# Optimization experiments

Hardware: AMD Instinct MI355X
Metric: run time of the kernel (lower is better)

The kernel has to match this reference:

```python
import jax, jax.numpy as jnp
import numpy as np

TAU = 0.01
MASK_VALUE = -1000000.0


def setup_inputs() -> dict:
    key = jax.random.key(0)
    kq, kk, km, k1, k2, k3 = jax.random.split(key, 6)
    B, Lq, Lk = 4, 512, 512
    Dq = Dk = 256
    H = 128
    queries = jax.random.normal(kq, (B, Lq, Dq), dtype=jnp.float32)
    keys = jax.random.normal(kk, (B, Lk, Dk), dtype=jnp.float32)
    # valid length along the size-2 logits axis, in {1, 2}
    mask = jax.random.randint(km, (B, Lq, Lk), 1, 3, dtype=jnp.int32)
    Wq = jax.random.normal(k1, (H, Dq), dtype=jnp.float32) * 0.05
    Wk = jax.random.normal(k2, (H, Dk), dtype=jnp.float32) * 0.05
    Wv = jax.random.normal(k3, (2, H), dtype=jnp.float32) * 0.05
    return {"queries": queries, "keys": keys, "mask": mask,
            "Wq": Wq, "Wk": Wk, "Wv": Wv}


def reference(queries, keys, mask, Wq, Wk, Wv):
    # Linear projections (no bias): [B,Lq,H], [B,Lk,H]
    q = jnp.einsum('bqd,hd->bqh', queries, Wq)
    k = jnp.einsum('bkd,hd->bkh', keys, Wk)
    # Bahdanau broadcast-add + tanh: [B,Lq,Lk,H]
    features = jnp.tanh(q[:, :, None, :] + k[:, None, :, :])
    # Project to 2 logits: [B,Lq,Lk,2]
    scores = jnp.einsum('bqkh,ch->bqkc', features, Wv)
    # sequence_mask along the size-2 last axis: positions >= valid_len get -1e6
    pos = jnp.arange(2, dtype=mask.dtype)
    masked = jnp.where(pos < mask[..., None], scores, MASK_VALUE)
    # Gumbel-softmax (soft), tau=0.01, over last axis; take channel 0
    g = jax.random.gumbel(jax.random.key(42), masked.shape, dtype=masked.dtype)
    weights = jax.nn.softmax((masked + g) / TAU, axis=-1)
    return weights[..., 0]
```

## Files before the change

### kernel.cpp

```cpp
#include <hip/hip_runtime.h>
#include <stdint.h>


#define BB 4
#define LLEN 512
#define DD 256
#define HH 128

#define TWO_LOG2E 2.8853900817779268f
#define LOG2E_100 144.26950408889634f

#define NWAVES 2048
#define REGION 512

__device__ __forceinline__ uint32_t rotl32(uint32_t v, int r) {
  return __builtin_amdgcn_alignbit(v, v, 32 - r);
}

__device__ __forceinline__ void tf2x32(uint32_t x0, uint32_t x1,
                                       uint32_t& o0, uint32_t& o1) {
  const uint32_t k0 = 0u;
  const uint32_t k1 = 42u;
  const uint32_t k2 = 0x1BD11BDAu ^ k0 ^ k1;

  x0 += k0; x1 += k1;
#define TFR(r) { x0 += x1; x1 = rotl32(x1, (r)); x1 ^= x0; }
  TFR(13) TFR(15) TFR(26) TFR(6)
  x0 += k1; x1 += k2 + 1u;
  TFR(17) TFR(29) TFR(16) TFR(24)
  x0 += k2; x1 += k0 + 2u;
  TFR(13) TFR(15) TFR(26) TFR(6)
  x0 += k0; x1 += k1 + 3u;
  TFR(17) TFR(29) TFR(16) TFR(24)
  x0 += k1; x1 += k2 + 4u;
  TFR(13) TFR(15) TFR(26) TFR(6)
  x0 += k2; x1 += k0 + 5u;
#undef TFR
  o0 = x0; o1 = x1;
}

__device__ __forceinline__ float jax_u01(uint32_t flat) {
  uint32_t o0, o1;
  tf2x32(0u, flat, o0, o1);
  const uint32_t bits = o0 ^ o1;
  const float f = __uint_as_float((bits >> 9) | 0x3F800000u) - 1.0f;
  return fmaxf(f, 1.17549435e-38f);
}

__global__ __launch_bounds__(128) void proj_kernel(
    const float* __restrict__ queries, const float* __restrict__ keys,
    const float* __restrict__ Wq, const float* __restrict__ Wk,
    float* __restrict__ EQ, float* __restrict__ EK) {
  const int blk = blockIdx.x;
  const bool isK = blk >= 512;
  const int rb = (isK ? blk - 512 : blk) * 4;
  const float* __restrict__ in = isK ? keys : queries;
  const float* __restrict__ W  = isK ? Wk : Wq;
  float* __restrict__ outp     = isK ? EK : EQ;

  __shared__ float rows[4][DD];
  const float4* in4 = reinterpret_cast<const float4*>(in + (size_t)rb * DD);
  float4* rows4 = reinterpret_cast<float4*>(&rows[0][0]);
  #pragma unroll
  for (int t = threadIdx.x; t < 4 * DD / 4; t += 128) rows4[t] = in4[t];
  __syncthreads();

  const int h = threadIdx.x;
  const float4* W4 = reinterpret_cast<const float4*>(W + (size_t)h * DD);
  float a0 = 0.f, a1 = 0.f, a2 = 0.f, a3 = 0.f;
  #pragma unroll 8
  for (int d4 = 0; d4 < DD / 4; ++d4) {
    const float4 w = W4[d4];
    const int d = d4 * 4;
    a0 = fmaf(w.x, rows[0][d], fmaf(w.y, rows[0][d+1], fmaf(w.z, rows[0][d+2], fmaf(w.w, rows[0][d+3], a0))));
    a1 = fmaf(w.x, rows[1][d], fmaf(w.y, rows[1][d+1], fmaf(w.z, rows[1][d+2], fmaf(w.w, rows[1][d+3], a1))));
    a2 = fmaf(w.x, rows[2][d], fmaf(w.y, rows[2][d+1], fmaf(w.z, rows[2][d+2], fmaf(w.w, rows[2][d+3], a2))));
    a3 = fmaf(w.x, rows[3][d], fmaf(w.y, rows[3][d+1], fmaf(w.z, rows[3][d+2], fmaf(w.w, rows[3][d+3], a3))));
  }
  float* orow = outp + (size_t)rb * HH + h;
  orow[0 * HH] = __builtin_amdgcn_exp2f(a0 * TWO_LOG2E);
  orow[1 * HH] = __builtin_amdgcn_exp2f(a1 * TWO_LOG2E);
  orow[2 * HH] = __builtin_amdgcn_exp2f(a2 * TWO_LOG2E);
  orow[3 * HH] = __builtin_amdgcn_exp2f(a3 * TWO_LOG2E);
}

#define GRP(accv, qv, kv, wd) {                                       \
    float4 A_;                                                        \
    A_.x = fmaf((qv).x, (kv).x, 1.0f);                                \
    A_.y = fmaf((qv).y, (kv).y, 1.0f);                                \
    A_.z = fmaf((qv).z, (kv).z, 1.0f);                                \
    A_.w = fmaf((qv).w, (kv).w, 1.0f);                                \
    const float p01_ = A_.x * A_.y;                                   \
    const float p23_ = A_.z * A_.w;                                   \
    const float n01_ = fmaf((wd).x, A_.y, (wd).y * A_.x);             \
    const float n23_ = fmaf((wd).z, A_.w, (wd).w * A_.z);             \
    const float num_ = fmaf(n01_, p23_, n23_ * p01_);                 \
    const float rc_  = __builtin_amdgcn_rcpf(p01_ * p23_);            \
    (accv) = fmaf(num_, rc_, (accv)); }

__global__ __launch_bounds__(256) void attn_loop(
    const float* __restrict__ EQ, const float* __restrict__ EK,
    const int* __restrict__ mask, const float* __restrict__ Wv,
    float* __restrict__ out, uint32_t* __restrict__ counts,
    uint2* __restrict__ entbuf) {
  __shared__ float4 QL[32][33];
  __shared__ float4 KL[64][33];
  __shared__ float4 wdL[32];

  const int bi = blockIdx.x, bj = blockIdx.y, b = blockIdx.z;
  const int i0 = bi * 32, j0 = bj * 64;

  const float4* Q4 = reinterpret_cast<const float4*>(EQ) + ((size_t)b * LLEN + i0) * (HH / 4);
  const float4* K4 = reinterpret_cast<const float4*>(EK) + ((size_t)b * LLEN + j0) * (HH / 4);
  for (int t = threadIdx.x; t < 1024 + 2048; t += 256) {
    if (t < 1024) {
      QL[t >> 5][t & 31] = Q4[t];
    } else {
      const int u = t - 1024;
      KL[u >> 5][u & 31] = K4[u];
    }
  }
  if (threadIdx.x < 32) {
    const float4 w0 = reinterpret_cast<const float4*>(Wv)[threadIdx.x];
    const float4 w1 = reinterpret_cast<const float4*>(Wv)[32 + threadIdx.x];
    float4 wd; wd.x = w0.x - w1.x; wd.y = w0.y - w1.y;
    wd.z = w0.z - w1.z; wd.w = w0.w - w1.w;
    wdL[threadIdx.x] = wd;
  }
  __syncthreads();

  const int jj = threadIdx.x & 31;
  const int ib = threadIdx.x >> 5;

  const uint32_t row0 = (uint32_t)b * LLEN + i0 + ib;
  const uint32_t col0 = j0 + jj;
  int mreg[4][2];
  #pragma unroll
  for (int r = 0; r < 4; ++r)
    #pragma unroll
    for (int c = 0; c < 2; ++c)
      mreg[r][c] = mask[(row0 + 8u * r) * LLEN + col0 + 32u * c];

  float Swd = 0.f;
  #pragma unroll
  for (int t = 0; t < 32; ++t) {
    const float4 wd = wdL[t];
    Swd += (wd.x + wd.y) + (wd.z + wd.w);
  }

  float acc[4][2] = {{0.f,0.f},{0.f,0.f},{0.f,0.f},{0.f,0.f}};

  #pragma unroll 4
  for (int h4 = 0; h4 < HH / 4; ++h4) {
    const float4 kv0 = KL[jj][h4];
    const float4 kv1 = KL[jj + 32][h4];
    const float4 wd  = wdL[h4];
    const float4 qv0 = QL[ib][h4];
    const float4 qv1 = QL[ib + 8][h4];
    const float4 qv2 = QL[ib + 16][h4];
    const float4 qv3 = QL[ib + 24][h4];
    GRP(acc[0][0], qv0, kv0, wd) GRP(acc[0][1], qv0, kv1, wd)
    GRP(acc[1][0], qv1, kv0, wd) GRP(acc[1][1], qv1, kv1, wd)
    GRP(acc[2][0], qv2, kv0, wd) GRP(acc[2][1], qv2, kv1, wd)
    GRP(acc[3][0], qv3, kv0, wd) GRP(acc[3][1], qv3, kv1, wd)
  }

  const int lane = threadIdx.x & 63;
  const unsigned long long lanemask_lt = (1ull << lane) - 1ull;
  const uint32_t wave_id =
      (((uint32_t)blockIdx.z * gridDim.y + blockIdx.y) * gridDim.x + blockIdx.x) * 4u
      + (threadIdx.x >> 6);
  uint2* __restrict__ reg = entbuf + (size_t)wave_id * REGION;

  uint32_t off = 0;
  #pragma unroll
  for (int r = 0; r < 4; ++r) {
    #pragma unroll
    for (int c = 0; c < 2; ++c) {
      const uint32_t idx = (row0 + 8u * r) * LLEN + col0 + 32u * c;
      const bool need = (mreg[r][c] >= 2);
      const unsigned long long bal = __ballot(need);
      if (need) {
        const uint32_t rank = (uint32_t)__popcll(bal & lanemask_lt);
        uint2 ent;
        ent.x = idx;
        ent.y = __float_as_uint(fmaf(-2.0f, acc[r][c], Swd));
        reg[off + rank] = ent;
      } else {
        out[idx] = 1.0f;
      }
      off += (uint32_t)__popcll(bal);
    }
  }
  if (lane == 0) counts[wave_id] = off;
}

__global__ __launch_bounds__(256) void attn_epi(
    const uint32_t* __restrict__ counts, const uint2* __restrict__ entbuf,
    float* __restrict__ out) {
  const int lane = threadIdx.x & 63;
  const uint32_t g = (uint32_t)blockIdx.x * 4u + (threadIdx.x >> 6);
  const uint32_t cnt = counts[g];
  if (cnt == 0) return;
  const uint2* __restrict__ reg = entbuf + (size_t)g * REGION;

  const int iters = (int)((cnt + 63u) >> 6);
  #pragma unroll 2
  for (int k = 0; k < iters; ++k) {
    const uint32_t e = (uint32_t)k * 64u + (uint32_t)lane;
    const bool valid = e < cnt;
    const uint32_t eL = valid ? e : (cnt - 1u);
    const uint2 ent = reg[eL];

    const float dv = __uint_as_float(ent.y);
    const float l0 = __log2f(jax_u01(ent.x * 2u));
    const float l1 = __log2f(jax_u01(ent.x * 2u + 1u));
    const float rl = l1 * __builtin_amdgcn_rcpf(l0);
    const float dl = __log2f(rl);
    const float t  = fmaf(dv, LOG2E_100, 100.0f * dl);
    const float o  = __builtin_amdgcn_rcpf(1.0f + __builtin_amdgcn_exp2f(-t));
    if (valid) out[ent.x] = o;
  }
}

extern "C" void kernel_launch(void* const* d_in, const int* in_sizes, int n_in,
                              void* d_out, int out_size, void* d_ws, size_t ws_size,
                              hipStream_t stream) {
  const float* queries = (const float*)d_in[0];
  const float* keys    = (const float*)d_in[1];
  const int*   mask    = (const int*)d_in[2];
  const float* Wq      = (const float*)d_in[3];
  const float* Wk      = (const float*)d_in[4];
  const float* Wv      = (const float*)d_in[5];
  float* out = (float*)d_out;

  float* EQ = (float*)d_ws;
  float* EK = EQ + (size_t)BB * LLEN * HH;
  uint32_t* counts = (uint32_t*)(EK + (size_t)BB * LLEN * HH);
  uint2* entbuf = (uint2*)((char*)counts + 16384);

  proj_kernel<<<dim3(1024), dim3(128), 0, stream>>>(
      queries, keys, Wq, Wk, EQ, EK);
  attn_loop<<<dim3(LLEN / 32, LLEN / 64, BB), dim3(256), 0, stream>>>(
      EQ, EK, mask, Wv, out, counts, entbuf);
  attn_epi<<<dim3(NWAVES / 4), dim3(256), 0, stream>>>(
      counts, entbuf, out);
}
```

Measured before the change: 47.22 us.

## Precompute Gumbel noise in the projection kernel and drop the compaction epilogue

Gumbel noise log terms for all sites are now computed in extra blocks of the projection kernel and written to a workspace buffer. The attention kernel reads that buffer alongside the mask and computes the final sigmoid inline, which removes the ballot/compaction scatter and the third epilogue launch. In exchange, threefry hashing now runs for every site rather than only the roughly half whose mask is 2. It also adds a 4 MB write and a 4 MB read of noise values.

Result: faster. 42.13 us (-10.8%).

```diff
diff --git a/kernel.cpp b/kernel.cpp
--- a/kernel.cpp
+++ b/kernel.cpp
@@ -10,8 +10,8 @@
 #define TWO_LOG2E 2.8853900817779268f
 #define LOG2E_100 144.26950408889634f
 
-#define NWAVES 2048
-#define REGION 512
+#define NSITES (BB * LLEN * LLEN)
+#define GUMBEL_THREADS (NSITES / 2)
 
 __device__ __forceinline__ uint32_t rotl32(uint32_t v, int r) {
   return __builtin_amdgcn_alignbit(v, v, 32 - r);
@@ -47,11 +47,25 @@
   return fmaxf(f, 1.17549435e-38f);
 }
 
-__global__ __launch_bounds__(128) void proj_kernel(
+__global__ __launch_bounds__(128) void prep_kernel(
     const float* __restrict__ queries, const float* __restrict__ keys,
     const float* __restrict__ Wq, const float* __restrict__ Wk,
-    float* __restrict__ EQ, float* __restrict__ EK) {
+    float* __restrict__ EQ, float* __restrict__ EK, float* __restrict__ G) {
   const int blk = blockIdx.x;
+
+  if (blk >= 1024) {
+    const uint32_t base = (uint32_t)(blk - 1024) * 128u + threadIdx.x;
+    #pragma unroll
+    for (int rep = 0; rep < 2; ++rep) {
+      const uint32_t s = base + (uint32_t)rep * GUMBEL_THREADS;
+      const float l0 = __log2f(jax_u01(s * 2u));
+      const float l1 = __log2f(jax_u01(s * 2u + 1u));
+      const float rl = l1 * __builtin_amdgcn_rcpf(l0);
+      G[s] = 100.0f * __log2f(rl);
+    }
+    return;
+  }
+
   const bool isK = blk >= 512;
   const int rb = (isK ? blk - 512 : blk) * 4;
   const float* __restrict__ in = isK ? keys : queries;
@@ -98,11 +112,10 @@
     const float rc_  = __builtin_amdgcn_rcpf(p01_ * p23_);            \
     (accv) = fmaf(num_, rc_, (accv)); }
 
-__global__ __launch_bounds__(256) void attn_loop(
+__global__ __launch_bounds__(256) void attn_kernel(
     const float* __restrict__ EQ, const float* __restrict__ EK,
     const int* __restrict__ mask, const float* __restrict__ Wv,
-    float* __restrict__ out, uint32_t* __restrict__ counts,
-    uint2* __restrict__ entbuf) {
+    const float* __restrict__ G, float* __restrict__ out) {
   __shared__ float4 QL[32][33];
   __shared__ float4 KL[64][33];
   __shared__ float4 wdL[32];
@@ -134,12 +147,16 @@
 
   const uint32_t row0 = (uint32_t)b * LLEN + i0 + ib;
   const uint32_t col0 = j0 + jj;
-  int mreg[4][2];
+  int   mreg[4][2];
+  float greg[4][2];
   #pragma unroll
   for (int r = 0; r < 4; ++r)
     #pragma unroll
-    for (int c = 0; c < 2; ++c)
-      mreg[r][c] = mask[(row0 + 8u * r) * LLEN + col0 + 32u * c];
+    for (int c = 0; c < 2; ++c) {
+      const uint32_t idx = (row0 + 8u * r) * LLEN + col0 + 32u * c;
+      mreg[r][c] = mask[idx];
+      greg[r][c] = G[idx];
+    }
 
   float Swd = 0.f;
   #pragma unroll
@@ -165,61 +182,16 @@
     GRP(acc[3][0], qv3, kv0, wd) GRP(acc[3][1], qv3, kv1, wd)
   }
 
-  const int lane = threadIdx.x & 63;
-  const unsigned long long lanemask_lt = (1ull << lane) - 1ull;
-  const uint32_t wave_id =
-      (((uint32_t)blockIdx.z * gridDim.y + blockIdx.y) * gridDim.x + blockIdx.x) * 4u
-      + (threadIdx.x >> 6);
-  uint2* __restrict__ reg = entbuf + (size_t)wave_id * REGION;
-
-  uint32_t off = 0;
   #pragma unroll
   for (int r = 0; r < 4; ++r) {
     #pragma unroll
     for (int c = 0; c < 2; ++c) {
       const uint32_t idx = (row0 + 8u * r) * LLEN + col0 + 32u * c;
-      const bool need = (mreg[r][c] >= 2);
-      const unsigned long long bal = __ballot(need);
-      if (need) {
-        const uint32_t rank = (uint32_t)__popcll(bal & lanemask_lt);
-        uint2 ent;
-        ent.x = idx;
-        ent.y = __float_as_uint(fmaf(-2.0f, acc[r][c], Swd));
-        reg[off + rank] = ent;
-      } else {
-        out[idx] = 1.0f;
-      }
-      off += (uint32_t)__popcll(bal);
-    }
-  }
-  if (lane == 0) counts[wave_id] = off;
-}
-
-__global__ __launch_bounds__(256) void attn_epi(
-    const uint32_t* __restrict__ counts, const uint2* __restrict__ entbuf,
-    float* __restrict__ out) {
-  const int lane = threadIdx.x & 63;
-  const uint32_t g = (uint32_t)blockIdx.x * 4u + (threadIdx.x >> 6);
-  const uint32_t cnt = counts[g];
-  if (cnt == 0) return;
-  const uint2* __restrict__ reg = entbuf + (size_t)g * REGION;
-
-  const int iters = (int)((cnt + 63u) >> 6);
-  #pragma unroll 2
-  for (int k = 0; k < iters; ++k) {
-    const uint32_t e = (uint32_t)k * 64u + (uint32_t)lane;
-    const bool valid = e < cnt;
-    const uint32_t eL = valid ? e : (cnt - 1u);
-    const uint2 ent = reg[eL];
-
-    const float dv = __uint_as_float(ent.y);
-    const float l0 = __log2f(jax_u01(ent.x * 2u));
-    const float l1 = __log2f(jax_u01(ent.x * 2u + 1u));
-    const float rl = l1 * __builtin_amdgcn_rcpf(l0);
-    const float dl = __log2f(rl);
-    const float t  = fmaf(dv, LOG2E_100, 100.0f * dl);
-    const float o  = __builtin_amdgcn_rcpf(1.0f + __builtin_amdgcn_exp2f(-t));
-    if (valid) out[ent.x] = o;
+      const float d_ = fmaf(-2.0f, acc[r][c], Swd);
+      const float t_ = fmaf(d_, LOG2E_100, greg[r][c]);
+      const float o_ = __builtin_amdgcn_rcpf(1.0f + __builtin_amdgcn_exp2f(-t_));
+      out[idx] = (mreg[r][c] >= 2) ? o_ : 1.0f;
+    }
   }
 }
 
@@ -236,13 +208,10 @@
 
   float* EQ = (float*)d_ws;
   float* EK = EQ + (size_t)BB * LLEN * HH;
-  uint32_t* counts = (uint32_t*)(EK + (size_t)BB * LLEN * HH);
-  uint2* entbuf = (uint2*)((char*)counts + 16384);
-
-  proj_kernel<<<dim3(1024), dim3(128), 0, stream>>>(
-      queries, keys, Wq, Wk, EQ, EK);
-  attn_loop<<<dim3(LLEN / 32, LLEN / 64, BB), dim3(256), 0, stream>>>(
-      EQ, EK, mask, Wv, out, counts, entbuf);
-  attn_epi<<<dim3(NWAVES / 4), dim3(256), 0, stream>>>(
-      counts, entbuf, out);
-}
+  float* G  = EK + (size_t)BB * LLEN * HH;
+
+  prep_kernel<<<dim3(1024 + GUMBEL_THREADS / 128), dim3(128), 0, stream>>>(
+      queries, keys, Wq, Wk, EQ, EK, G);
+  attn_kernel<<<dim3(LLEN / 32, LLEN / 64, BB), dim3(256), 0, stream>>>(
+      EQ, EK, mask, Wv, G, out);
+}
```
